# Kernel optimization log

Measured on AMD Instinct MI355X. Metric: run time of the kernel, lower is better.

The kernel has to match this reference:

```python
import jax, jax.numpy as jnp
import numpy as np

N_WIRES = 10
DIM = 1 << N_WIRES  # 1024
EPS = 1e-12

_CNOT = jnp.array([[1, 0, 0, 0],
                   [0, 1, 0, 0],
                   [0, 0, 0, 1],
                   [0, 0, 1, 0]], dtype=jnp.complex64)

# signs[i, j] = (-1)^{bit_j(i)} for single-Z Pauli string on wire j (qubit 0 = MSB)
_bits = (np.arange(DIM)[:, None] >> (N_WIRES - 1 - np.arange(N_WIRES))[None, :]) & 1
_Z_SIGNS = jnp.asarray(1.0 - 2.0 * _bits, dtype=jnp.float32)  # (DIM, N_WIRES)


def _rx_gate(theta):
    c = jnp.cos(theta / 2).astype(jnp.complex64)
    s = jnp.sin(theta / 2).astype(jnp.complex64)
    return jnp.stack([jnp.stack([c, -1j * s]), jnp.stack([-1j * s, c])])


def _ry_gate(theta):
    c = jnp.cos(theta / 2).astype(jnp.complex64)
    s = jnp.sin(theta / 2).astype(jnp.complex64)
    return jnp.stack([jnp.stack([c, -s]), jnp.stack([s, c])])


def _apply_1q(psi, gate, q):
    # psi: (N, DIM) complex64; apply 2x2 gate on qubit q (qubit 0 = MSB)
    N = psi.shape[0]
    left, right = 1 << q, 1 << (N_WIRES - 1 - q)
    psi = psi.reshape(N, left, 2, right)
    psi = jnp.einsum('ab,nxby->nxay', gate, psi)
    return psi.reshape(N, DIM)


def _apply_2q(psi, gate, q0, q1):
    # gate: (4,4) acting on qubits (q0, q1) in that order
    G = gate.reshape(2, 2, 2, 2)
    if q0 > q1:
        G = jnp.transpose(G, (1, 0, 3, 2))
        q0, q1 = q1, q0
    N = psi.shape[0]
    a = 1 << q0
    b = 1 << (q1 - q0 - 1)
    c = 1 << (N_WIRES - 1 - q1)
    psi = psi.reshape(N, a, 2, b, 2, c)
    psi = jnp.einsum('ijkl,nxkylz->nxiyjz', G, psi)
    return psi.reshape(N, DIM)


def setup_inputs() -> dict:
    key = jax.random.key(0)
    k1, k2, k3, k4 = jax.random.split(key, 4)
    x = jax.random.normal(k1, (4, 1024, DIM), dtype=jnp.float32)
    rx0 = jax.random.normal(k2, (N_WIRES,), dtype=jnp.float32)
    ry0 = jax.random.normal(k3, (N_WIRES,), dtype=jnp.float32)
    ry1 = jax.random.normal(k4, (N_WIRES,), dtype=jnp.float32)
    return {"x": x, "rx0": rx0, "ry0": ry0, "ry1": ry1}


def reference(x, rx0, ry0, ry1):
    B, T, C = x.shape
    x_flat = x.reshape(B * T, C)
    # amplitude encoding: L2-normalize each row into a complex state vector
    norm = jnp.linalg.norm(x_flat, axis=1, keepdims=True)
    psi = (x_flat / jnp.maximum(norm, EPS)).astype(jnp.complex64)  # (N, DIM)
    # layer 1: RX then RY on each wire
    for j in range(N_WIRES):
        psi = _apply_1q(psi, _rx_gate(rx0[j]), j)
        psi = _apply_1q(psi, _ry_gate(ry0[j]), j)
    # CNOT ring
    for j in range(N_WIRES):
        psi = _apply_2q(psi, _CNOT, j, (j + 1) % N_WIRES)
    # layer 2: RY on each wire
    for j in range(N_WIRES):
        psi = _apply_1q(psi, _ry_gate(ry1[j]), j)
    # expectation values of Z on each wire: sum_i |psi_i|^2 * (-1)^{bit_j(i)}
    probs = psi.real ** 2 + psi.imag ** 2  # (N, DIM) float32
    out = probs @ _Z_SIGNS                  # (N, N_WIRES)
    return out.reshape(B, T, N_WIRES).astype(jnp.float32)
```

## Files before the change

kernel.cpp:

```cpp
#include <hip/hip_runtime.h>

#define NW 10
typedef float f32x2 __attribute__((ext_vector_type(2)));

__device__ __forceinline__ int gperm(int v) {
    #pragma unroll
    for (int k = 9; k >= 0; --k) {
        const int cs = 9 - k;
        const int ts = 9 - ((k + 1) % NW);
        v ^= ((v >> cs) & 1) << ts;
    }
    return v;
}

__device__ __forceinline__ int PQ(int i) {
    return i + ((i >> 4) << 1) + ((i >> 8) << 1);
}
#define PBUF 1156

__device__ __forceinline__ float rl(float v, int lane) {
    return __int_as_float(__builtin_amdgcn_readlane(__float_as_int(v), lane));
}

template<int SH>
__device__ __forceinline__ void cgp(float* re, float* im,
                                    float ar, float ai, float br, float bi) {
    #pragma unroll
    for (int base = 0; base < 16; base += (2 << SH)) {
        #pragma unroll
        for (int off = 0; off < (1 << SH); off += 2) {
            const int r0 = base + off, r1 = r0 + (1 << SH);
            const f32x2 v0r = {re[r0], re[r0+1]}, v0i = {im[r0], im[r0+1]};
            const f32x2 v1r = {re[r1], re[r1+1]}, v1i = {im[r1], im[r1+1]};
            const f32x2 n0r = ar*v0r - ai*v0i + br*v1r - bi*v1i;
            const f32x2 n0i = ar*v0i + ai*v0r + br*v1i + bi*v1r;
            const f32x2 n1r = ar*v1r + ai*v1i - br*v0r - bi*v0i;
            const f32x2 n1i = ar*v1i - ai*v1r - br*v0i + bi*v0r;
            re[r0]=n0r.x; re[r0+1]=n0r.y; im[r0]=n0i.x; im[r0+1]=n0i.y;
            re[r1]=n1r.x; re[r1+1]=n1r.y; im[r1]=n1i.x; im[r1+1]=n1i.y;
        }
    }
}

__device__ __forceinline__ void cg0(float* re, float* im,
                                    float ar, float ai, float br, float bi) {
    #pragma unroll
    for (int r = 0; r < 16; r += 2) {
        const float v0r = re[r], v0i = im[r], v1r = re[r+1], v1i = im[r+1];
        re[r]   =  ar*v0r - ai*v0i + br*v1r - bi*v1i;
        im[r]   =  ar*v0i + ai*v0r + br*v1i + bi*v1r;
        re[r+1] = -br*v0r - bi*v0i + ar*v1r + ai*v1i;
        im[r+1] =  bi*v0r - br*v0i + ar*v1i - ai*v1r;
    }
}

template<int SH>
__device__ __forceinline__ void rgp(float* re, float* im, float c, float s) {
    #pragma unroll
    for (int base = 0; base < 16; base += (2 << SH)) {
        #pragma unroll
        for (int off = 0; off < (1 << SH); off += 2) {
            const int r0 = base + off, r1 = r0 + (1 << SH);
            const f32x2 v0r = {re[r0], re[r0+1]}, v0i = {im[r0], im[r0+1]};
            const f32x2 v1r = {re[r1], re[r1+1]}, v1i = {im[r1], im[r1+1]};
            const f32x2 n0r = c*v0r - s*v1r, n0i = c*v0i - s*v1i;
            const f32x2 n1r = s*v0r + c*v1r, n1i = s*v0i + c*v1i;
            re[r0]=n0r.x; re[r0+1]=n0r.y; im[r0]=n0i.x; im[r0+1]=n0i.y;
            re[r1]=n1r.x; re[r1+1]=n1r.y; im[r1]=n1i.x; im[r1+1]=n1i.y;
        }
    }
}

__device__ __forceinline__ void rg0(float* re, float* im, float c, float s) {
    #pragma unroll
    for (int r = 0; r < 16; r += 2) {
        const float v0r = re[r], v0i = im[r], v1r = re[r+1], v1i = im[r+1];
        re[r]   = c*v0r - s*v1r;  im[r]   = c*v0i - s*v1i;
        re[r+1] = s*v0r + c*v1r;  im[r+1] = s*v0i + c*v1i;
    }
}

__global__ __launch_bounds__(64) void qsa_main(
    const float* __restrict__ x,
    const float* __restrict__ rx0,
    const float* __restrict__ ry0,
    const float* __restrict__ ry1,
    float* __restrict__ out) {

    __shared__ __align__(16) float2 sp[PBUF];

    const int t = threadIdx.x;
    const int n = blockIdx.x;

    float re[16], im[16];
    const float* xr = x + ((size_t)n << 10) + (t << 4);
    #pragma unroll
    for (int r = 0; r < 16; r += 4) {
        const float4 v = *reinterpret_cast<const float4*>(xr + r);
        re[r] = v.x; re[r+1] = v.y; re[r+2] = v.z; re[r+3] = v.w;
    }

    float car = 0.f, cai = 0.f, cbr = 0.f, cbi = 0.f, cc1 = 0.f, cs1 = 0.f;
    if (t < NW) {
        float sx, cx, sy0, cy0;
        sincosf(0.5f * rx0[t], &sx,  &cx);
        sincosf(0.5f * ry0[t], &sy0, &cy0);
        sincosf(0.5f * ry1[t], &cs1, &cc1);
        car =  cy0 * cx;  cai =  sy0 * sx;
        cbr = -sy0 * cx;  cbi = -cy0 * sx;
    }

    float ss = 0.f;
    #pragma unroll
    for (int r = 0; r < 16; ++r) ss += re[r] * re[r];
    #pragma unroll
    for (int b = 32; b > 0; b >>= 1) ss += __shfl_xor(ss, b, 64);
    const float scale = 1.0f / fmaxf(sqrtf(ss), 1e-12f);

    {
        const float ar = rl(car,9), ai = rl(cai,9), br = rl(cbr,9), bi = rl(cbi,9);
        #pragma unroll
        for (int r = 0; r < 16; r += 4) {
            const f32x2 v0 = {re[r] * scale,   re[r+2] * scale};
            const f32x2 v1 = {re[r+1] * scale, re[r+3] * scale};
            const f32x2 n0r = ar*v0 + br*v1, n0i = ai*v0 + bi*v1;
            const f32x2 n1r = ar*v1 - br*v0, n1i = bi*v0 - ai*v1;
            re[r]   = n0r.x; im[r]   = n0i.x; re[r+1] = n1r.x; im[r+1] = n1i.x;
            re[r+2] = n0r.y; im[r+2] = n0i.y; re[r+3] = n1r.y; im[r+3] = n1i.y;
        }
    }
    cgp<1>(re, im, rl(car,8), rl(cai,8), rl(cbr,8), rl(cbi,8));
    cgp<2>(re, im, rl(car,7), rl(cai,7), rl(cbr,7), rl(cbi,7));
    cgp<3>(re, im, rl(car,6), rl(cai,6), rl(cbr,6), rl(cbi,6));

    #pragma unroll
    for (int r = 0; r < 16; r += 2)
        *reinterpret_cast<float4*>(&sp[PQ((t << 4) | r)]) =
            make_float4(re[r], im[r], re[r+1], im[r+1]);
    __syncthreads();
    {
        const int b0 = ((t >> 4) << 8) | (t & 15);
        #pragma unroll
        for (int r = 0; r < 16; ++r) {
            const float2 v = sp[PQ(b0 + (r << 4))];
            re[r] = v.x; im[r] = v.y;
        }
    }

    cg0   (re, im, rl(car,5), rl(cai,5), rl(cbr,5), rl(cbi,5));
    cgp<1>(re, im, rl(car,4), rl(cai,4), rl(cbr,4), rl(cbi,4));
    cgp<2>(re, im, rl(car,3), rl(cai,3), rl(cbr,3), rl(cbi,3));
    cgp<3>(re, im, rl(car,2), rl(cai,2), rl(cbr,2), rl(cbi,2));

    {
        const int b0 = ((t >> 4) << 8) | (t & 15);
        #pragma unroll
        for (int r = 0; r < 16; ++r)
            sp[PQ(b0 + (r << 4))] = make_float2(re[r], im[r]);
    }
    __syncthreads();
    #pragma unroll
    for (int r = 0; r < 16; r += 2) {
        const int i = ((r >> 2) << 8) | (t << 2) | (r & 3);
        const float4 q = *reinterpret_cast<const float4*>(&sp[PQ(i)]);
        re[r] = q.x; im[r] = q.y; re[r+1] = q.z; im[r+1] = q.w;
    }

    cgp<2>(re, im, rl(car,1), rl(cai,1), rl(cbr,1), rl(cbi,1));
    cgp<3>(re, im, rl(car,0), rl(cai,0), rl(cbr,0), rl(cbi,0));

    #pragma unroll
    for (int r = 0; r < 16; r += 2) {
        const int i = ((r >> 2) << 8) | (t << 2) | (r & 3);
        *reinterpret_cast<float4*>(&sp[PQ(i)]) =
            make_float4(re[r], im[r], re[r+1], im[r+1]);
    }
    __syncthreads();
    {
        const int gt = gperm(t << 4);
        #pragma unroll
        for (int r = 0; r < 16; ++r) {
            const float2 v = sp[PQ(gt ^ gperm(r))];
            re[r] = v.x; im[r] = v.y;
        }
    }

    rg0   (re, im, rl(cc1,9), rl(cs1,9));
    rgp<1>(re, im, rl(cc1,8), rl(cs1,8));
    rgp<2>(re, im, rl(cc1,7), rl(cs1,7));
    rgp<3>(re, im, rl(cc1,6), rl(cs1,6));

    #pragma unroll
    for (int r = 0; r < 16; r += 2)
        *reinterpret_cast<float4*>(&sp[PQ((t << 4) | r)]) =
            make_float4(re[r], im[r], re[r+1], im[r+1]);
    __syncthreads();
    {
        const int b0 = ((t >> 4) << 8) | (t & 15);
        #pragma unroll
        for (int r = 0; r < 16; ++r) {
            const float2 v = sp[PQ(b0 + (r << 4))];
            re[r] = v.x; im[r] = v.y;
        }
    }

    rg0   (re, im, rl(cc1,5), rl(cs1,5));
    rgp<1>(re, im, rl(cc1,4), rl(cs1,4));
    rgp<2>(re, im, rl(cc1,3), rl(cs1,3));
    rgp<3>(re, im, rl(cc1,2), rl(cs1,2));

    {
        const int b0 = ((t >> 4) << 8) | (t & 15);
        #pragma unroll
        for (int r = 0; r < 16; ++r)
            sp[PQ(b0 + (r << 4))] = make_float2(re[r], im[r]);
    }
    __syncthreads();
    #pragma unroll
    for (int r = 0; r < 16; r += 2) {
        const int i = ((r >> 2) << 8) | (t << 2) | (r & 3);
        const float4 q = *reinterpret_cast<const float4*>(&sp[PQ(i)]);
        re[r] = q.x; im[r] = q.y; re[r+1] = q.z; im[r+1] = q.w;
    }

    rgp<2>(re, im, rl(cc1,1), rl(cs1,1));
    rgp<3>(re, im, rl(cc1,0), rl(cs1,0));

    float P = 0.f, a0 = 0.f, a1 = 0.f, a8 = 0.f, a9 = 0.f;
    #pragma unroll
    for (int r = 0; r < 16; ++r) {
        const float p = re[r] * re[r] + im[r] * im[r];
        P  += p;
        a0 += (r & 8) ? -p : p;
        a1 += (r & 4) ? -p : p;
        a8 += (r & 2) ? -p : p;
        a9 += (r & 1) ? -p : p;
    }
    #pragma unroll
    for (int b = 1; b < 64; b <<= 1) {
        a0 += __shfl_xor(a0, b, 64);
        a1 += __shfl_xor(a1, b, 64);
        a8 += __shfl_xor(a8, b, 64);
        a9 += __shfl_xor(a9, b, 64);
        const float e = __shfl_xor(P, b, 64);
        P = (t & b) ? (e - P) : (e + P);
    }
    float* o = out + (size_t)n * NW;
    if (t == 0) { o[0] = a0; o[1] = a1; o[8] = a8; o[9] = a9; }
    if (t == 32) o[2] = P;
    if (t == 16) o[3] = P;
    if (t ==  8) o[4] = P;
    if (t ==  4) o[5] = P;
    if (t ==  2) o[6] = P;
    if (t ==  1) o[7] = P;
}

extern "C" void kernel_launch(void* const* d_in, const int* in_sizes, int n_in,
                              void* d_out, int out_size, void* d_ws, size_t ws_size,
                              hipStream_t stream) {
    const float* x   = (const float*)d_in[0];
    const float* rx0 = (const float*)d_in[1];
    const float* ry0 = (const float*)d_in[2];
    const float* ry1 = (const float*)d_in[3];
    float* out = (float*)d_out;
    const int nstates = in_sizes[0] >> 10;
    qsa_main<<<nstates, 64, 0, stream>>>(x, rx0, ry0, ry1, out);
}
```

Measured before the change: 82.13 us.

## Split LDS into separate real/imag planes and vectorize gates with packed f32x2

Stores the state as paired f32x2 registers so each gate update maps to packed FP32 math, including the adjacent-pair gates through lane swaps. Shared memory is split into separate real and imaginary arrays with a new padding function. Because the write-back now reuses the buffers just read, extra barriers are added before each write. The aim is fewer ALU instructions through packed math and fewer LDS bank conflicts, at the cost of more barriers and more scalar LDS accesses on the strided phases.

Result: no change. 81.48 us (-0.8%).

```diff
diff --git a/kernel.cpp b/kernel.cpp
--- a/kernel.cpp
+++ b/kernel.cpp
@@ -2,6 +2,10 @@
 
 #define NW 10
 typedef float f32x2 __attribute__((ext_vector_type(2)));
+
+__device__ __forceinline__ f32x2 swap2(f32x2 v) {
+    return __builtin_shufflevector(v, v, 1, 0);
+}
 
 __device__ __forceinline__ int gperm(int v) {
     #pragma unroll
@@ -13,70 +17,66 @@
     return v;
 }
 
-__device__ __forceinline__ int PQ(int i) {
-    return i + ((i >> 4) << 1) + ((i >> 8) << 1);
-}
-#define PBUF 1156
+__device__ __forceinline__ int PF(int i) {
+    return i + ((i >> 5) << 2) + ((i >> 8) << 3);
+}
+#define PBUF 1176
 
 __device__ __forceinline__ float rl(float v, int lane) {
     return __int_as_float(__builtin_amdgcn_readlane(__float_as_int(v), lane));
 }
 
-template<int SH>
-__device__ __forceinline__ void cgp(float* re, float* im,
+template<int D>
+__device__ __forceinline__ void cgv(f32x2* rf, f32x2* mf,
                                     float ar, float ai, float br, float bi) {
     #pragma unroll
-    for (int base = 0; base < 16; base += (2 << SH)) {
-        #pragma unroll
-        for (int off = 0; off < (1 << SH); off += 2) {
-            const int r0 = base + off, r1 = r0 + (1 << SH);
-            const f32x2 v0r = {re[r0], re[r0+1]}, v0i = {im[r0], im[r0+1]};
-            const f32x2 v1r = {re[r1], re[r1+1]}, v1i = {im[r1], im[r1+1]};
-            const f32x2 n0r = ar*v0r - ai*v0i + br*v1r - bi*v1i;
-            const f32x2 n0i = ar*v0i + ai*v0r + br*v1i + bi*v1r;
-            const f32x2 n1r = ar*v1r + ai*v1i - br*v0r - bi*v0i;
-            const f32x2 n1i = ar*v1i - ai*v1r - br*v0i + bi*v0r;
-            re[r0]=n0r.x; re[r0+1]=n0r.y; im[r0]=n0i.x; im[r0+1]=n0i.y;
-            re[r1]=n1r.x; re[r1+1]=n1r.y; im[r1]=n1i.x; im[r1+1]=n1i.y;
-        }
-    }
-}
-
-__device__ __forceinline__ void cg0(float* re, float* im,
-                                    float ar, float ai, float br, float bi) {
-    #pragma unroll
-    for (int r = 0; r < 16; r += 2) {
-        const float v0r = re[r], v0i = im[r], v1r = re[r+1], v1i = im[r+1];
-        re[r]   =  ar*v0r - ai*v0i + br*v1r - bi*v1i;
-        im[r]   =  ar*v0i + ai*v0r + br*v1i + bi*v1r;
-        re[r+1] = -br*v0r - bi*v0i + ar*v1r + ai*v1i;
-        im[r+1] =  bi*v0r - br*v0i + ar*v1i - ai*v1r;
-    }
-}
-
-template<int SH>
-__device__ __forceinline__ void rgp(float* re, float* im, float c, float s) {
-    #pragma unroll
-    for (int base = 0; base < 16; base += (2 << SH)) {
-        #pragma unroll
-        for (int off = 0; off < (1 << SH); off += 2) {
-            const int r0 = base + off, r1 = r0 + (1 << SH);
-            const f32x2 v0r = {re[r0], re[r0+1]}, v0i = {im[r0], im[r0+1]};
-            const f32x2 v1r = {re[r1], re[r1+1]}, v1i = {im[r1], im[r1+1]};
-            const f32x2 n0r = c*v0r - s*v1r, n0i = c*v0i - s*v1i;
-            const f32x2 n1r = s*v0r + c*v1r, n1i = s*v0i + c*v1i;
-            re[r0]=n0r.x; re[r0+1]=n0r.y; im[r0]=n0i.x; im[r0+1]=n0i.y;
-            re[r1]=n1r.x; re[r1+1]=n1r.y; im[r1]=n1i.x; im[r1+1]=n1i.y;
-        }
-    }
-}
-
-__device__ __forceinline__ void rg0(float* re, float* im, float c, float s) {
-    #pragma unroll
-    for (int r = 0; r < 16; r += 2) {
-        const float v0r = re[r], v0i = im[r], v1r = re[r+1], v1i = im[r+1];
-        re[r]   = c*v0r - s*v1r;  im[r]   = c*v0i - s*v1i;
-        re[r+1] = s*v0r + c*v1r;  im[r+1] = s*v0i + c*v1i;
+    for (int base = 0; base < 8; base += 2 * D) {
+        #pragma unroll
+        for (int off = 0; off < D; ++off) {
+            const int j0 = base + off, j1 = j0 + D;
+            const f32x2 v0r = rf[j0], v0i = mf[j0];
+            const f32x2 v1r = rf[j1], v1i = mf[j1];
+            rf[j0] = ar*v0r - ai*v0i + br*v1r - bi*v1i;
+            mf[j0] = ar*v0i + ai*v0r + br*v1i + bi*v1r;
+            rf[j1] = ar*v1r + ai*v1i - br*v0r - bi*v0i;
+            mf[j1] = ar*v1i - ai*v1r - br*v0i + bi*v0r;
+        }
+    }
+}
+
+__device__ __forceinline__ void cgv0(f32x2* rf, f32x2* mf,
+                                     float ar, float ai, float br, float bi) {
+    const f32x2 aiN = {-ai,  ai};
+    const f32x2 brN = { br, -br};
+    #pragma unroll
+    for (int j = 0; j < 8; ++j) {
+        const f32x2 vr = rf[j], vi = mf[j];
+        rf[j] = ar*vr + aiN*vi + brN*swap2(vr) - bi*swap2(vi);
+        mf[j] = ar*vi - aiN*vr + brN*swap2(vi) + bi*swap2(vr);
+    }
+}
+
+template<int D>
+__device__ __forceinline__ void rgv(f32x2* rf, f32x2* mf, float c, float s) {
+    #pragma unroll
+    for (int base = 0; base < 8; base += 2 * D) {
+        #pragma unroll
+        for (int off = 0; off < D; ++off) {
+            const int j0 = base + off, j1 = j0 + D;
+            const f32x2 v0r = rf[j0], v0i = mf[j0];
+            const f32x2 v1r = rf[j1], v1i = mf[j1];
+            rf[j0] = c*v0r - s*v1r;  mf[j0] = c*v0i - s*v1i;
+            rf[j1] = s*v0r + c*v1r;  mf[j1] = s*v0i + c*v1i;
+        }
+    }
+}
+
+__device__ __forceinline__ void rgv0(f32x2* rf, f32x2* mf, float c, float s) {
+    const f32x2 sN = {-s, s};
+    #pragma unroll
+    for (int j = 0; j < 8; ++j) {
+        rf[j] = c*rf[j] + sN*swap2(rf[j]);
+        mf[j] = c*mf[j] + sN*swap2(mf[j]);
     }
 }
 
@@ -87,17 +87,19 @@
     const float* __restrict__ ry1,
     float* __restrict__ out) {
 
-    __shared__ __align__(16) float2 sp[PBUF];
+    __shared__ __align__(16) float reb[PBUF];
+    __shared__ __align__(16) float imb[PBUF];
 
     const int t = threadIdx.x;
     const int n = blockIdx.x;
 
-    float re[16], im[16];
+    f32x2 rf[8], mf[8];
     const float* xr = x + ((size_t)n << 10) + (t << 4);
     #pragma unroll
-    for (int r = 0; r < 16; r += 4) {
-        const float4 v = *reinterpret_cast<const float4*>(xr + r);
-        re[r] = v.x; re[r+1] = v.y; re[r+2] = v.z; re[r+3] = v.w;
+    for (int k = 0; k < 4; ++k) {
+        const float4 v = *reinterpret_cast<const float4*>(xr + 4 * k);
+        rf[2*k]   = f32x2{v.x, v.y};
+        rf[2*k+1] = f32x2{v.z, v.w};
     }
 
     float car = 0.f, cai = 0.f, cbr = 0.f, cbi = 0.f, cc1 = 0.f, cs1 = 0.f;
@@ -110,132 +112,165 @@
         cbr = -sy0 * cx;  cbi = -cy0 * sx;
     }
 
-    float ss = 0.f;
-    #pragma unroll
-    for (int r = 0; r < 16; ++r) ss += re[r] * re[r];
+    f32x2 ssv = {0.f, 0.f};
+    #pragma unroll
+    for (int j = 0; j < 8; ++j) ssv += rf[j] * rf[j];
+    float ss = ssv.x + ssv.y;
     #pragma unroll
     for (int b = 32; b > 0; b >>= 1) ss += __shfl_xor(ss, b, 64);
     const float scale = 1.0f / fmaxf(sqrtf(ss), 1e-12f);
 
     {
         const float ar = rl(car,9), ai = rl(cai,9), br = rl(cbr,9), bi = rl(cbi,9);
-        #pragma unroll
-        for (int r = 0; r < 16; r += 4) {
-            const f32x2 v0 = {re[r] * scale,   re[r+2] * scale};
-            const f32x2 v1 = {re[r+1] * scale, re[r+3] * scale};
-            const f32x2 n0r = ar*v0 + br*v1, n0i = ai*v0 + bi*v1;
-            const f32x2 n1r = ar*v1 - br*v0, n1i = bi*v0 - ai*v1;
-            re[r]   = n0r.x; im[r]   = n0i.x; re[r+1] = n1r.x; im[r+1] = n1i.x;
-            re[r+2] = n0r.y; im[r+2] = n0i.y; re[r+3] = n1r.y; im[r+3] = n1i.y;
-        }
-    }
-    cgp<1>(re, im, rl(car,8), rl(cai,8), rl(cbr,8), rl(cbi,8));
-    cgp<2>(re, im, rl(car,7), rl(cai,7), rl(cbr,7), rl(cbi,7));
-    cgp<3>(re, im, rl(car,6), rl(cai,6), rl(cbr,6), rl(cbi,6));
-
-    #pragma unroll
-    for (int r = 0; r < 16; r += 2)
-        *reinterpret_cast<float4*>(&sp[PQ((t << 4) | r)]) =
-            make_float4(re[r], im[r], re[r+1], im[r+1]);
+        const f32x2 brN = {br, -br};
+        const f32x2 aiP = {ai, -ai};
+        #pragma unroll
+        for (int j = 0; j < 8; ++j) {
+            const f32x2 v = scale * rf[j];
+            rf[j] = ar*v  + brN*swap2(v);
+            mf[j] = aiP*v + bi*swap2(v);
+        }
+    }
+    cgv<1>(rf, mf, rl(car,8), rl(cai,8), rl(cbr,8), rl(cbi,8));
+    cgv<2>(rf, mf, rl(car,7), rl(cai,7), rl(cbr,7), rl(cbi,7));
+    cgv<4>(rf, mf, rl(car,6), rl(cai,6), rl(cbr,6), rl(cbi,6));
+
+    #pragma unroll
+    for (int k = 0; k < 4; ++k) {
+        const int p = PF((t << 4) + 4 * k);
+        *reinterpret_cast<float4*>(&reb[p]) =
+            make_float4(rf[2*k].x, rf[2*k].y, rf[2*k+1].x, rf[2*k+1].y);
+        *reinterpret_cast<float4*>(&imb[p]) =
+            make_float4(mf[2*k].x, mf[2*k].y, mf[2*k+1].x, mf[2*k+1].y);
+    }
     __syncthreads();
     {
         const int b0 = ((t >> 4) << 8) | (t & 15);
         #pragma unroll
-        for (int r = 0; r < 16; ++r) {
-            const float2 v = sp[PQ(b0 + (r << 4))];
-            re[r] = v.x; im[r] = v.y;
-        }
-    }
-
-    cg0   (re, im, rl(car,5), rl(cai,5), rl(cbr,5), rl(cbi,5));
-    cgp<1>(re, im, rl(car,4), rl(cai,4), rl(cbr,4), rl(cbi,4));
-    cgp<2>(re, im, rl(car,3), rl(cai,3), rl(cbr,3), rl(cbi,3));
-    cgp<3>(re, im, rl(car,2), rl(cai,2), rl(cbr,2), rl(cbi,2));
-
+        for (int j = 0; j < 8; ++j) {
+            const int p0 = PF(b0 + ((2*j) << 4)), p1 = PF(b0 + ((2*j+1) << 4));
+            rf[j] = f32x2{reb[p0], reb[p1]};
+            mf[j] = f32x2{imb[p0], imb[p1]};
+        }
+    }
+
+    cgv0  (rf, mf, rl(car,5), rl(cai,5), rl(cbr,5), rl(cbi,5));
+    cgv<1>(rf, mf, rl(car,4), rl(cai,4), rl(cbr,4), rl(cbi,4));
+    cgv<2>(rf, mf, rl(car,3), rl(cai,3), rl(cbr,3), rl(cbi,3));
+    cgv<4>(rf, mf, rl(car,2), rl(cai,2), rl(cbr,2), rl(cbi,2));
+
+    __syncthreads();
     {
         const int b0 = ((t >> 4) << 8) | (t & 15);
         #pragma unroll
-        for (int r = 0; r < 16; ++r)
-            sp[PQ(b0 + (r << 4))] = make_float2(re[r], im[r]);
-    }
-    __syncthreads();
-    #pragma unroll
-    for (int r = 0; r < 16; r += 2) {
-        const int i = ((r >> 2) << 8) | (t << 2) | (r & 3);
-        const float4 q = *reinterpret_cast<const float4*>(&sp[PQ(i)]);
-        re[r] = q.x; im[r] = q.y; re[r+1] = q.z; im[r+1] = q.w;
-    }
-
-    cgp<2>(re, im, rl(car,1), rl(cai,1), rl(cbr,1), rl(cbi,1));
-    cgp<3>(re, im, rl(car,0), rl(cai,0), rl(cbr,0), rl(cbi,0));
-
-    #pragma unroll
-    for (int r = 0; r < 16; r += 2) {
-        const int i = ((r >> 2) << 8) | (t << 2) | (r & 3);
-        *reinterpret_cast<float4*>(&sp[PQ(i)]) =
-            make_float4(re[r], im[r], re[r+1], im[r+1]);
+        for (int j = 0; j < 8; ++j) {
+            const int p0 = PF(b0 + ((2*j) << 4)), p1 = PF(b0 + ((2*j+1) << 4));
+            reb[p0] = rf[j].x; reb[p1] = rf[j].y;
+            imb[p0] = mf[j].x; imb[p1] = mf[j].y;
+        }
+    }
+    __syncthreads();
+    #pragma unroll
+    for (int k = 0; k < 4; ++k) {
+        const int p = PF((k << 8) | (t << 2));
+        const float4 qr = *reinterpret_cast<const float4*>(&reb[p]);
+        const float4 qi = *reinterpret_cast<const float4*>(&imb[p]);
+        rf[2*k] = f32x2{qr.x, qr.y}; rf[2*k+1] = f32x2{qr.z, qr.w};
+        mf[2*k] = f32x2{qi.x, qi.y}; mf[2*k+1] = f32x2{qi.z, qi.w};
+    }
+
+    cgv<2>(rf, mf, rl(car,1), rl(cai,1), rl(cbr,1), rl(cbi,1));
+    cgv<4>(rf, mf, rl(car,0), rl(cai,0), rl(cbr,0), rl(cbi,0));
+
+    __syncthreads();
+    #pragma unroll
+    for (int k = 0; k < 4; ++k) {
+        const int p = PF((k << 8) | (t << 2));
+        *reinterpret_cast<float4*>(&reb[p]) =
+            make_float4(rf[2*k].x, rf[2*k].y, rf[2*k+1].x, rf[2*k+1].y);
+        *reinterpret_cast<float4*>(&imb[p]) =
+            make_float4(mf[2*k].x, mf[2*k].y, mf[2*k+1].x, mf[2*k+1].y);
     }
     __syncthreads();
     {
         const int gt = gperm(t << 4);
         #pragma unroll
-        for (int r = 0; r < 16; ++r) {
-            const float2 v = sp[PQ(gt ^ gperm(r))];
-            re[r] = v.x; im[r] = v.y;
-        }
-    }
-
-    rg0   (re, im, rl(cc1,9), rl(cs1,9));
-    rgp<1>(re, im, rl(cc1,8), rl(cs1,8));
-    rgp<2>(re, im, rl(cc1,7), rl(cs1,7));
-    rgp<3>(re, im, rl(cc1,6), rl(cs1,6));
-
-    #pragma unroll
-    for (int r = 0; r < 16; r += 2)
-        *reinterpret_cast<float4*>(&sp[PQ((t << 4) | r)]) =
-            make_float4(re[r], im[r], re[r+1], im[r+1]);
+        for (int j = 0; j < 8; ++j) {
+            const int p0 = PF(gt ^ gperm(2*j)), p1 = PF(gt ^ gperm(2*j+1));
+            rf[j] = f32x2{reb[p0], reb[p1]};
+            mf[j] = f32x2{imb[p0], imb[p1]};
+        }
+    }
+
+    rgv0  (rf, mf, rl(cc1,9), rl(cs1,9));
+    rgv<1>(rf, mf, rl(cc1,8), rl(cs1,8));
+    rgv<2>(rf, mf, rl(cc1,7), rl(cs1,7));
+    rgv<4>(rf, mf, rl(cc1,6), rl(cs1,6));
+
+    __syncthreads();
+    #pragma unroll
+    for (int k = 0; k < 4; ++k) {
+        const int p = PF((t << 4) + 4 * k);
+        *reinterpret_cast<float4*>(&reb[p]) =
+            make_float4(rf[2*k].x, rf[2*k].y, rf[2*k+1].x, rf[2*k+1].y);
+        *reinterpret_cast<float4*>(&imb[p]) =
+            make_float4(mf[2*k].x, mf[2*k].y, mf[2*k+1].x, mf[2*k+1].y);
+    }
     __syncthreads();
     {
         const int b0 = ((t >> 4) << 8) | (t & 15);
         #pragma unroll
-        for (int r = 0; r < 16; ++r) {
-            const float2 v = sp[PQ(b0 + (r << 4))];
-            re[r] = v.x; im[r] = v.y;
-        }
-    }
-
-    rg0   (re, im, rl(cc1,5), rl(cs1,5));
-    rgp<1>(re, im, rl(cc1,4), rl(cs1,4));
-    rgp<2>(re, im, rl(cc1,3), rl(cs1,3));
-    rgp<3>(re, im, rl(cc1,2), rl(cs1,2));
-
+        for (int j = 0; j < 8; ++j) {
+            const int p0 = PF(b0 + ((2*j) << 4)), p1 = PF(b0 + ((2*j+1) << 4));
+            rf[j] = f32x2{reb[p0], reb[p1]};
+            mf[j] = f32x2{imb[p0], imb[p1]};
+        }
+    }
+
+    rgv0  (rf, mf, rl(cc1,5), rl(cs1,5));
+    rgv<1>(rf, mf, rl(cc1,4), rl(cs1,4));
+    rgv<2>(rf, mf, rl(cc1,3), rl(cs1,3));
+    rgv<4>(rf, mf, rl(cc1,2), rl(cs1,2));
+
+    __syncthreads();
     {
         const int b0 = ((t >> 4) << 8) | (t & 15);
         #pragma unroll
-        for (int r = 0; r < 16; ++r)
-            sp[PQ(b0 + (r << 4))] = make_float2(re[r], im[r]);
-    }
-    __syncthreads();
-    #pragma unroll
-    for (int r = 0; r < 16; r += 2) {
-        const int i = ((r >> 2) << 8) | (t << 2) | (r & 3);
-        const float4 q = *reinterpret_cast<const float4*>(&sp[PQ(i)]);
-        re[r] = q.x; im[r] = q.y; re[r+1] = q.z; im[r+1] = q.w;
-    }
-
-    rgp<2>(re, im, rl(cc1,1), rl(cs1,1));
-    rgp<3>(re, im, rl(cc1,0), rl(cs1,0));
-
-    float P = 0.f, a0 = 0.f, a1 = 0.f, a8 = 0.f, a9 = 0.f;
-    #pragma unroll
-    for (int r = 0; r < 16; ++r) {
-        const float p = re[r] * re[r] + im[r] * im[r];
-        P  += p;
-        a0 += (r & 8) ? -p : p;
-        a1 += (r & 4) ? -p : p;
-        a8 += (r & 2) ? -p : p;
-        a9 += (r & 1) ? -p : p;
-    }
+        for (int j = 0; j < 8; ++j) {
+            const int p0 = PF(b0 + ((2*j) << 4)), p1 = PF(b0 + ((2*j+1) << 4));
+            reb[p0] = rf[j].x; reb[p1] = rf[j].y;
+            imb[p0] = mf[j].x; imb[p1] = mf[j].y;
+        }
+    }
+    __syncthreads();
+    #pragma unroll
+    for (int k = 0; k < 4; ++k) {
+        const int p = PF((k << 8) | (t << 2));
+        const float4 qr = *reinterpret_cast<const float4*>(&reb[p]);
+        const float4 qi = *reinterpret_cast<const float4*>(&imb[p]);
+        rf[2*k] = f32x2{qr.x, qr.y}; rf[2*k+1] = f32x2{qr.z, qr.w};
+        mf[2*k] = f32x2{qi.x, qi.y}; mf[2*k+1] = f32x2{qi.z, qi.w};
+    }
+
+    rgv<2>(rf, mf, rl(cc1,1), rl(cs1,1));
+    rgv<4>(rf, mf, rl(cc1,0), rl(cs1,0));
+
+    f32x2 accP = {0,0}, acc9 = {0,0}, acc8 = {0,0}, acc1 = {0,0}, acc0 = {0,0};
+    const f32x2 pm = {1.f, -1.f};
+    #pragma unroll
+    for (int j = 0; j < 8; ++j) {
+        const f32x2 p = rf[j]*rf[j] + mf[j]*mf[j];
+        accP += p;
+        acc9 += pm * p;
+        if (j & 1) acc8 -= p; else acc8 += p;
+        if (j & 2) acc1 -= p; else acc1 += p;
+        if (j & 4) acc0 -= p; else acc0 += p;
+    }
+    float P  = accP.x + accP.y;
+    float a9 = acc9.x + acc9.y;
+    float a8 = acc8.x + acc8.y;
+    float a1 = acc1.x + acc1.y;
+    float a0 = acc0.x + acc0.y;
     #pragma unroll
     for (int b = 1; b < 64; b <<= 1) {
         a0 += __shfl_xor(a0, b, 64);
```
